# Kernel tuning notes

Hardware: AMD Instinct MI355X
Metric: run time of the kernel (lower is better)

The kernel has to match this reference:

```python
import jax, jax.numpy as jnp
import numpy as np

N = 100000        # nodes
E = 1600000       # edges (avg degree 16)
F_IN = 512        # num_features
H1, D1 = 8, 8     # layer-1 heads x per-head dim (concat -> 64)
C = 16            # num_classes (layer-2: 1 head, dim C)
NEG_SLOPE = 0.2


def setup_inputs() -> dict:
    key = jax.random.key(0)
    ks = jax.random.split(key, 8)
    x = jax.random.normal(ks[0], (N, F_IN), dtype=jnp.float32)
    edge_index = jax.random.randint(ks[1], (2, E), 0, N, dtype=jnp.int64)
    W1 = jax.random.normal(ks[2], (F_IN, H1 * D1), dtype=jnp.float32) / np.float32(np.sqrt(F_IN))
    a1_src = jax.random.normal(ks[3], (H1, D1), dtype=jnp.float32) * 0.1
    a1_dst = jax.random.normal(ks[4], (H1, D1), dtype=jnp.float32) * 0.1
    W2 = jax.random.normal(ks[5], (H1 * D1, C), dtype=jnp.float32) / np.float32(np.sqrt(H1 * D1))
    a2_src = jax.random.normal(ks[6], (1, C), dtype=jnp.float32) * 0.1
    a2_dst = jax.random.normal(ks[7], (1, C), dtype=jnp.float32) * 0.1
    return {"x": x, "edge_index": edge_index, "W1": W1, "a1_src": a1_src,
            "a1_dst": a1_dst, "W2": W2, "a2_src": a2_src, "a2_dst": a2_dst}


def gat_layer(x, src, dst, W, a_s, a_d, heads, out_dim):
    """Multi-head GAT conv: gather -> per-edge leaky-relu score -> segment
    softmax over destination -> scatter-aggregate. Returns [N, heads, out_dim]."""
    n = x.shape[0]
    h = (x @ W).reshape(n, heads, out_dim)            # [N, H, D]
    es = jnp.einsum('nhd,hd->nh', h, a_s)             # source attention term
    ed = jnp.einsum('nhd,hd->nh', h, a_d)             # dest attention term
    e = jax.nn.leaky_relu(es[src] + ed[dst], NEG_SLOPE)   # [E, H]
    m = jax.ops.segment_max(e, dst, num_segments=n)       # stable softmax max
    ex = jnp.exp(e - m[dst])
    s = jax.ops.segment_sum(ex, dst, num_segments=n)
    alpha = ex / s[dst]                               # [E, H]
    out = jax.ops.segment_sum(h[src] * alpha[..., None], dst, num_segments=n)
    return out                                        # [N, H, D]


def reference(x, edge_index, W1, a1_src, a1_dst, W2, a2_src, a2_dst):
    n = x.shape[0]
    loop = jnp.arange(n, dtype=edge_index.dtype)
    src = jnp.concatenate([edge_index[0], loop])      # add self-loops
    dst = jnp.concatenate([edge_index[1], loop])
    # eval mode: dropout(p=0.6, training=False) is identity
    h1 = gat_layer(x, src, dst, W1, a1_src, a1_dst, H1, D1).reshape(n, H1 * D1)
    h1 = jax.nn.elu(h1)
    h2 = gat_layer(h1, src, dst, W2, a2_src, a2_dst, 1, C).reshape(n, C)
    return jax.nn.log_softmax(h2, axis=1)
```

## Files before the change

kernel.cpp:

```cpp
#include <hip/hip_runtime.h>
#include <hip/hip_bf16.h>

#define F_IN 512
#define H1 8
#define D1 8
#define F_MID 64
#define C 16
#define NEG_SLOPE 0.2f
#define SCAN_CHUNK 1024
#define BIN_CHUNK 8192
#define NB_MAX 1024
#define BUCKET_SHIFT 7
#define BUCKET_STRIDE 3072

typedef __attribute__((ext_vector_type(8))) short bf16x8;
typedef __attribute__((ext_vector_type(4))) float f32x4;

static __device__ __forceinline__ unsigned short f2bf(float f) {
    __hip_bfloat16 h = __float2bfloat16(f);
    return *(unsigned short*)&h;
}

__global__ __launch_bounds__(256) void k_bin(const int* __restrict__ src,
                                             const int* __restrict__ dst,
                                             int* __restrict__ gcur,
                                             int2* __restrict__ bucketed,
                                             int n_edges, int nb) {
    __shared__ int cnt[NB_MAX];
    __shared__ int base[NB_MAX];
    const int t = threadIdx.x;
    const int eb = blockIdx.x * BIN_CHUNK;
    for (int b = t; b < nb; b += 256) cnt[b] = 0;
    __syncthreads();
#pragma unroll
    for (int i = 0; i < BIN_CHUNK / 256; ++i) {
        int e = eb + i * 256 + t;
        if (e < n_edges) atomicAdd(&cnt[dst[e] >> BUCKET_SHIFT], 1);
    }
    __syncthreads();
    for (int b = t; b < nb; b += 256) {
        int c = cnt[b];
        base[b] = c > 0 ? atomicAdd(&gcur[b], c) : 0;
        cnt[b] = 0;
    }
    __syncthreads();
#pragma unroll
    for (int i = 0; i < BIN_CHUNK / 256; ++i) {
        int e = eb + i * 256 + t;
        if (e < n_edges) {
            int d = dst[e];
            int b = d >> BUCKET_SHIFT;
            int local = atomicAdd(&cnt[b], 1);
            bucketed[(size_t)b * BUCKET_STRIDE + base[b] + local] = make_int2(src[e], d);
        }
    }
}

__global__ __launch_bounds__(256) void k_bhist(const int* __restrict__ gcur,
                                               const int2* __restrict__ bucketed,
                                               int* __restrict__ counts, int n_nodes) {
    __shared__ int cnt[1 << BUCKET_SHIFT];
    const int t = threadIdx.x;
    const int b = blockIdx.x;
    if (t < (1 << BUCKET_SHIFT)) cnt[t] = 0;
    __syncthreads();
    const int total = gcur[b];
    const int2* bp = bucketed + (size_t)b * BUCKET_STRIDE;
    for (int i = t; i < total; i += 256)
        atomicAdd(&cnt[bp[i].y & ((1 << BUCKET_SHIFT) - 1)], 1);
    __syncthreads();
    if (t < (1 << BUCKET_SHIFT)) {
        int node = (b << BUCKET_SHIFT) + t;
        if (node < n_nodes) counts[node] = cnt[t];
    }
}

__global__ __launch_bounds__(256) void k_bsort(const int* __restrict__ gcur,
                                               const int2* __restrict__ bucketed,
                                               int* __restrict__ cursor,
                                               int* __restrict__ sorted_src) {
    const int b = blockIdx.x;
    const int total = gcur[b];
    const int2* bp = bucketed + (size_t)b * BUCKET_STRIDE;
    for (int i = threadIdx.x; i < total; i += 256) {
        int2 ed = bp[i];
        int pos = atomicAdd(&cursor[ed.y], 1);
        sorted_src[pos] = ed.x;
    }
}

__global__ __launch_bounds__(256) void k_scan_reduce(const int* __restrict__ counts,
                                                     int* __restrict__ block_sums, int n) {
    const int t = threadIdx.x;
    const int base = blockIdx.x * SCAN_CHUNK + t * 4;
    int s = 0;
#pragma unroll
    for (int j = 0; j < 4; ++j) {
        int idx = base + j;
        if (idx < n) s += counts[idx];
    }
#pragma unroll
    for (int off = 1; off < 64; off <<= 1) s += __shfl_xor(s, off, 64);
    __shared__ int ws[4];
    if ((t & 63) == 0) ws[t >> 6] = s;
    __syncthreads();
    if (t == 0) block_sums[blockIdx.x] = ws[0] + ws[1] + ws[2] + ws[3];
}

__global__ __launch_bounds__(256) void k_scan_sums(int* __restrict__ block_sums,
                                                   int* __restrict__ block_offs,
                                                   int* __restrict__ row_start_last,
                                                   int nb) {
    __shared__ int sh[256];
    const int t = threadIdx.x;
    sh[t] = (t < nb) ? block_sums[t] : 0;
    __syncthreads();
#pragma unroll
    for (int d = 1; d < 256; d <<= 1) {
        int v = (t >= d) ? sh[t - d] : 0;
        __syncthreads();
        sh[t] += v;
        __syncthreads();
    }
    if (t < nb) block_offs[t] = sh[t] - block_sums[t];
    if (t == 255) *row_start_last = sh[255];
}

__global__ __launch_bounds__(256) void k_scan_apply(const int* __restrict__ counts,
                                                    const int* __restrict__ block_offs,
                                                    int* __restrict__ row_start,
                                                    int* __restrict__ cursor, int n) {
    const int t = threadIdx.x;
    const int base = blockIdx.x * SCAN_CHUNK + t * 4;
    int c[4];
#pragma unroll
    for (int j = 0; j < 4; ++j) c[j] = (base + j < n) ? counts[base + j] : 0;
    const int tsum = c[0] + c[1] + c[2] + c[3];
    int isc = tsum;
#pragma unroll
    for (int off = 1; off < 64; off <<= 1) {
        int v = __shfl_up(isc, off, 64);
        if ((t & 63) >= off) isc += v;
    }
    __shared__ int wsum[4];
    if ((t & 63) == 63) wsum[t >> 6] = isc;
    __syncthreads();
    int woff = 0;
    const int w = t >> 6;
    for (int i = 0; i < 4; ++i) if (i < w) woff += wsum[i];
    int off = block_offs[blockIdx.x] + woff + (isc - tsum);
#pragma unroll
    for (int j = 0; j < 4; ++j) {
        int idx = base + j;
        if (idx < n) { row_start[idx] = off; cursor[idx] = off; }
        off += c[j];
    }
}

__global__ __launch_bounds__(256) void k_w1t(const float* __restrict__ W1,
                                             __hip_bfloat16* __restrict__ w1t) {
    int idx = blockIdx.x * 256 + threadIdx.x;
    int k = idx >> 6, n = idx & 63;
    w1t[n * F_IN + k] = __float2bfloat16(W1[idx]);
}

__global__ __launch_bounds__(256) void k_gemm1(const float* __restrict__ x,
                                               const __hip_bfloat16* __restrict__ w1t,
                                               const float* __restrict__ a1s,
                                               const float* __restrict__ a1d,
                                               __hip_bfloat16* __restrict__ h1b,
                                               float* __restrict__ es1,
                                               float* __restrict__ ed1, int n_nodes) {
    __shared__ unsigned short Xs[64][72];
    __shared__ unsigned short Ws[64][72];
    __shared__ float sas[64], sad[64];
    const int t = threadIdx.x;
    if (t < 64) sas[t] = a1s[t];
    else if (t < 128) sad[t - 64] = a1d[t - 64];

    const int wv = t >> 6, l = t & 63;
    const int q = l >> 4, m16 = l & 15;
    const int rowbase = blockIdx.x * 64;

    const int sr = t >> 2, sf = t & 3;
    int gx = rowbase + sr;
    gx = gx < n_nodes ? gx : n_nodes - 1;
    const float* xrow = x + (size_t)gx * F_IN;
    const __hip_bfloat16* wrow = w1t + (size_t)sr * F_IN;

    f32x4 acc[4];
#pragma unroll
    for (int i = 0; i < 4; ++i) acc[i] = (f32x4){0.f, 0.f, 0.f, 0.f};

    for (int kt = 0; kt < F_IN; kt += 64) {
#pragma unroll
        for (int j = 0; j < 4; ++j) {
            float4 v = *(const float4*)(xrow + kt + sf * 16 + j * 4);
            ushort4 b;
            b.x = f2bf(v.x); b.y = f2bf(v.y); b.z = f2bf(v.z); b.w = f2bf(v.w);
            *(ushort4*)&Xs[sr][sf * 16 + j * 4] = b;
        }
#pragma unroll
        for (int j = 0; j < 2; ++j) {
            *(int4*)&Ws[sr][sf * 16 + j * 8] =
                *(const int4*)(wrow + kt + sf * 16 + j * 8);
        }
        __syncthreads();
#pragma unroll
        for (int kk = 0; kk < 2; ++kk) {
            bf16x8 bfrag = *(const bf16x8*)&Xs[wv * 16 + m16][kk * 32 + q * 8];
#pragma unroll
            for (int tn = 0; tn < 4; ++tn) {
                bf16x8 afrag = *(const bf16x8*)&Ws[tn * 16 + m16][kk * 32 + q * 8];
                acc[tn] = __builtin_amdgcn_mfma_f32_16x16x32_bf16(afrag, bfrag, acc[tn], 0, 0, 0);
            }
        }
        __syncthreads();
    }

    const int node = rowbase + wv * 16 + m16;
    const bool ok = node < n_nodes;
#pragma unroll
    for (int tn = 0; tn < 4; ++tn) {
        const f32x4 a = acc[tn];
        const int nw0 = tn * 16 + q * 4;
        float vs = a.x * sas[nw0] + a.y * sas[nw0 + 1] + a.z * sas[nw0 + 2] + a.w * sas[nw0 + 3];
        float vd = a.x * sad[nw0] + a.y * sad[nw0 + 1] + a.z * sad[nw0 + 2] + a.w * sad[nw0 + 3];
        vs += __shfl_xor(vs, 16, 64);
        vd += __shfl_xor(vd, 16, 64);
        if (ok) {
            ushort4 b;
            b.x = f2bf(a.x); b.y = f2bf(a.y); b.z = f2bf(a.z); b.w = f2bf(a.w);
            *(ushort4*)(h1b + (size_t)node * F_MID + nw0) = b;
            if ((q & 1) == 0) {
                const int head = 2 * tn + (q >> 1);
                es1[node * H1 + head] = vs;
                ed1[node * H1 + head] = vd;
            }
        }
    }
}

__global__ __launch_bounds__(256) void k_gather1(const int* __restrict__ row_start,
                                                 const int* __restrict__ sorted_src,
                                                 const __hip_bfloat16* __restrict__ h1b,
                                                 const float* __restrict__ es1,
                                                 const float* __restrict__ ed1,
                                                 float* __restrict__ h1, int n_nodes) {
    const int n = blockIdx.x * 4 + (threadIdx.x >> 6);
    if (n >= n_nodes) return;
    const int lane = threadIdx.x & 63;
    const int h = lane >> 3;
    const float edh = ed1[n * H1 + h];
    const int beg = row_start[n], end = row_start[n + 1];
    float acc = 0.f, den = 0.f;
    for (int base = beg; base < end; base += 64) {
        const int m = min(64, end - base);
        const int li = lane < m ? lane : (m - 1);
        const int myS = sorted_src[base + li];
        int j = 0;
        for (; j + 4 <= m; j += 4) {
            const int s0 = __shfl(myS, j, 64), s1 = __shfl(myS, j + 1, 64);
            const int s2 = __shfl(myS, j + 2, 64), s3 = __shfl(myS, j + 3, 64);
            float e0 = es1[s0 * H1 + h], e1 = es1[s1 * H1 + h];
            float e2 = es1[s2 * H1 + h], e3 = es1[s3 * H1 + h];
            const float f0 = __bfloat162float(h1b[(size_t)s0 * F_MID + lane]);
            const float f1 = __bfloat162float(h1b[(size_t)s1 * F_MID + lane]);
            const float f2 = __bfloat162float(h1b[(size_t)s2 * F_MID + lane]);
            const float f3 = __bfloat162float(h1b[(size_t)s3 * F_MID + lane]);
            e0 += edh; e1 += edh; e2 += edh; e3 += edh;
            e0 = e0 > 0.f ? e0 : NEG_SLOPE * e0;
            e1 = e1 > 0.f ? e1 : NEG_SLOPE * e1;
            e2 = e2 > 0.f ? e2 : NEG_SLOPE * e2;
            e3 = e3 > 0.f ? e3 : NEG_SLOPE * e3;
            const float w0 = __expf(e0), w1 = __expf(e1), w2 = __expf(e2), w3 = __expf(e3);
            acc += w0 * f0 + w1 * f1 + w2 * f2 + w3 * f3;
            den += (w0 + w1) + (w2 + w3);
        }
        for (; j < m; ++j) {
            const int s = __shfl(myS, j, 64);
            float ev = es1[s * H1 + h] + edh;
            ev = ev > 0.f ? ev : NEG_SLOPE * ev;
            const float w = __expf(ev);
            acc += w * __bfloat162float(h1b[(size_t)s * F_MID + lane]);
            den += w;
        }
    }
    float evs = es1[n * H1 + h] + edh;
    evs = evs > 0.f ? evs : NEG_SLOPE * evs;
    const float ws = __expf(evs);
    acc += ws * __bfloat162float(h1b[(size_t)n * F_MID + lane]);
    den += ws;
    float v = acc / den;
    v = v > 0.f ? v : expm1f(v);
    h1[(size_t)n * F_MID + lane] = v;
}

__global__ void k_gemm2(const float* __restrict__ h1, const float* __restrict__ W2,
                        const float* __restrict__ a2s, const float* __restrict__ a2d,
                        __hip_bfloat16* __restrict__ h2b, float* __restrict__ es2,
                        float* __restrict__ ed2, int n_nodes) {
    __shared__ float w2s[F_MID * C];
    __shared__ float h1s[16][F_MID + 1];
    const int t = threadIdx.x;
    const int nb = blockIdx.x * 16;
    for (int i = t; i < F_MID * C; i += 256) w2s[i] = W2[i];
    for (int i = t; i < 16 * F_MID; i += 256) {
        int r = i >> 6, k = i & 63;
        int n = nb + r;
        h1s[r][k] = h1[(size_t)(n < n_nodes ? n : n_nodes - 1) * F_MID + k];
    }
    __syncthreads();
    const int r = t >> 4, c = t & 15;
    const int n = nb + r;
    float acc = 0.f;
#pragma unroll
    for (int k = 0; k < F_MID; ++k) acc += h1s[r][k] * w2s[k * C + c];
    float vs = acc * a2s[c], vd = acc * a2d[c];
#pragma unroll
    for (int off = 1; off < 16; off <<= 1) {
        vs += __shfl_xor(vs, off, 64);
        vd += __shfl_xor(vd, off, 64);
    }
    if (n < n_nodes) {
        h2b[(size_t)n * C + c] = __float2bfloat16(acc);
        if (c == 0) { es2[n] = vs; ed2[n] = vd; }
    }
}

__global__ __launch_bounds__(256) void k_gather2(const int* __restrict__ row_start,
                                                 const int* __restrict__ sorted_src,
                                                 const __hip_bfloat16* __restrict__ h2b,
                                                 const float* __restrict__ es2,
                                                 const float* __restrict__ ed2,
                                                 float* __restrict__ out, int n_nodes) {
    const int n = blockIdx.x * 16 + (threadIdx.x >> 4);
    if (n >= n_nodes) return;
    const int lane = threadIdx.x & 63;
    const int c = lane & 15;
    const int g = lane >> 4;
    const float ed = ed2[n];
    const int beg = row_start[n], end = row_start[n + 1];
    float acc = 0.f, den = 0.f;
    for (int base = beg; base < end; base += 16) {
        const int m = min(16, end - base);
        const int li = c < m ? c : (m - 1);
        const int myS = sorted_src[base + li];
        int j = 0;
        for (; j + 4 <= m; j += 4) {
            const int s0 = __shfl(myS, g * 16 + j, 64), s1 = __shfl(myS, g * 16 + j + 1, 64);
            const int s2 = __shfl(myS, g * 16 + j + 2, 64), s3 = __shfl(myS, g * 16 + j + 3, 64);
            float e0 = es2[s0] + ed, e1 = es2[s1] + ed, e2 = es2[s2] + ed, e3 = es2[s3] + ed;
            const float f0 = __bfloat162float(h2b[(size_t)s0 * C + c]);
            const float f1 = __bfloat162float(h2b[(size_t)s1 * C + c]);
            const float f2 = __bfloat162float(h2b[(size_t)s2 * C + c]);
            const float f3 = __bfloat162float(h2b[(size_t)s3 * C + c]);
            e0 = e0 > 0.f ? e0 : NEG_SLOPE * e0;
            e1 = e1 > 0.f ? e1 : NEG_SLOPE * e1;
            e2 = e2 > 0.f ? e2 : NEG_SLOPE * e2;
            e3 = e3 > 0.f ? e3 : NEG_SLOPE * e3;
            const float w0 = __expf(e0), w1 = __expf(e1), w2 = __expf(e2), w3 = __expf(e3);
            acc += w0 * f0 + w1 * f1 + w2 * f2 + w3 * f3;
            den += (w0 + w1) + (w2 + w3);
        }
        for (; j < m; ++j) {
            const int s = __shfl(myS, g * 16 + j, 64);
            float ev = es2[s] + ed;
            ev = ev > 0.f ? ev : NEG_SLOPE * ev;
            const float w = __expf(ev);
            acc += w * __bfloat162float(h2b[(size_t)s * C + c]);
            den += w;
        }
    }
    float evs = es2[n] + ed;
    evs = evs > 0.f ? evs : NEG_SLOPE * evs;
    const float ws = __expf(evs);
    acc += ws * __bfloat162float(h2b[(size_t)n * C + c]);
    den += ws;
    const float v = acc / den;
    float mx = v;
#pragma unroll
    for (int off = 1; off < 16; off <<= 1) mx = fmaxf(mx, __shfl_xor(mx, off, 64));
    float se = __expf(v - mx);
#pragma unroll
    for (int off = 1; off < 16; off <<= 1) se += __shfl_xor(se, off, 64);
    out[(size_t)n * C + c] = v - mx - __logf(se);
}

extern "C" void kernel_launch(void* const* d_in, const int* in_sizes, int n_in,
                              void* d_out, int out_size, void* d_ws, size_t ws_size,
                              hipStream_t stream) {
    const float* x   = (const float*)d_in[0];
    const int*   ei  = (const int*)d_in[1];
    const float* W1  = (const float*)d_in[2];
    const float* a1s = (const float*)d_in[3];
    const float* a1d = (const float*)d_in[4];
    const float* W2  = (const float*)d_in[5];
    const float* a2s = (const float*)d_in[6];
    const float* a2d = (const float*)d_in[7];
    float* out = (float*)d_out;

    const int n_nodes = in_sizes[0] / F_IN;
    const int n_edges = in_sizes[1] / 2;
    const int* src = ei;
    const int* dst = ei + n_edges;
    const int n_scan_blocks = (n_nodes + SCAN_CHUNK - 1) / SCAN_CHUNK;
    const int nb = (n_nodes + (1 << BUCKET_SHIFT) - 1) >> BUCKET_SHIFT;

    float* fws = (float*)d_ws;
    float* es1 = fws;
    float* ed1 = es1 + (size_t)n_nodes * H1;
    float* h1  = ed1 + (size_t)n_nodes * H1;
    float* es2 = h1  + (size_t)n_nodes * F_MID;
    float* ed2 = es2 + n_nodes;
    __hip_bfloat16* h1b = (__hip_bfloat16*)(ed2 + n_nodes);
    __hip_bfloat16* h2b = h1b + (size_t)n_nodes * F_MID;
    __hip_bfloat16* w1t = h2b + (size_t)n_nodes * C;
    int* iws        = (int*)(w1t + F_IN * F_MID);
    int* counts     = iws;
    int* gcur       = counts + n_nodes;
    int* row_start  = gcur + NB_MAX;
    int* cursor     = row_start + n_nodes + 1;
    int* sorted_src = cursor + n_nodes;
    int* block_sums = sorted_src + n_edges;
    int* block_offs = block_sums + 256;
    int2* bucketed  = (int2*)(((uintptr_t)(block_offs + 256) + 15) & ~(uintptr_t)15);

    hipMemsetAsync(counts, 0, ((size_t)n_nodes + NB_MAX) * sizeof(int), stream);

    k_bin<<<(n_edges + BIN_CHUNK - 1) / BIN_CHUNK, 256, 0, stream>>>(src, dst, gcur, bucketed, n_edges, nb);
    k_bhist<<<nb, 256, 0, stream>>>(gcur, bucketed, counts, n_nodes);
    k_scan_reduce<<<n_scan_blocks, 256, 0, stream>>>(counts, block_sums, n_nodes);
    k_scan_sums<<<1, 256, 0, stream>>>(block_sums, block_offs, &row_start[n_nodes], n_scan_blocks);
    k_scan_apply<<<n_scan_blocks, 256, 0, stream>>>(counts, block_offs, row_start, cursor, n_nodes);
    k_bsort<<<nb, 256, 0, stream>>>(gcur, bucketed, cursor, sorted_src);

    k_w1t<<<(F_IN * F_MID) / 256, 256, 0, stream>>>(W1, w1t);
    k_gemm1<<<(n_nodes + 63) / 64, 256, 0, stream>>>(x, w1t, a1s, a1d, h1b, es1, ed1, n_nodes);
    k_gather1<<<(n_nodes + 3) / 4, 256, 0, stream>>>(row_start, sorted_src, h1b, es1, ed1, h1, n_nodes);

    k_gemm2<<<(n_nodes + 15) / 16, 256, 0, stream>>>(h1, W2, a2s, a2d, h2b, es2, ed2, n_nodes);
    k_gather2<<<(n_nodes + 15) / 16, 256, 0, stream>>>(row_start, sorted_src, h2b, es2, ed2, out, n_nodes);
}
```

Measured before the change: 535.2 us.

## Replace global CSR scan with per-bucket local scan and shared-memory placement

```diff
diff --git a/kernel.cpp b/kernel.cpp
--- a/kernel.cpp
+++ b/kernel.cpp
@@ -7,8 +7,7 @@
 #define F_MID 64
 #define C 16
 #define NEG_SLOPE 0.2f
-#define SCAN_CHUNK 1024
-#define BIN_CHUNK 8192
+#define BIN_CHUNK 4096
 #define NB_MAX 1024
 #define BUCKET_SHIFT 7
 #define BUCKET_STRIDE 3072
@@ -56,104 +55,68 @@
     }
 }
 
-__global__ __launch_bounds__(256) void k_bhist(const int* __restrict__ gcur,
+__global__ __launch_bounds__(1024) void k_bscan(const int* __restrict__ gcur,
+                                                int* __restrict__ bucket_base,
+                                                int* __restrict__ row_start_last,
+                                                int nb, int n_edges_total) {
+    __shared__ int sh[1024];
+    const int t = threadIdx.x;
+    const int v = (t < nb) ? gcur[t] : 0;
+    sh[t] = v;
+    __syncthreads();
+#pragma unroll
+    for (int d = 1; d < 1024; d <<= 1) {
+        int u = (t >= d) ? sh[t - d] : 0;
+        __syncthreads();
+        sh[t] += u;
+        __syncthreads();
+    }
+    if (t < nb) bucket_base[t] = sh[t] - v;
+    if (t == 0) *row_start_last = n_edges_total;
+}
+
+__global__ __launch_bounds__(256) void k_place(const int* __restrict__ gcur,
+                                               const int* __restrict__ bucket_base,
                                                const int2* __restrict__ bucketed,
-                                               int* __restrict__ counts, int n_nodes) {
+                                               int* __restrict__ row_start,
+                                               int* __restrict__ sorted_src, int n_nodes) {
+    __shared__ int2 stage[BUCKET_STRIDE];
     __shared__ int cnt[1 << BUCKET_SHIFT];
+    __shared__ int cur[1 << BUCKET_SHIFT];
     const int t = threadIdx.x;
     const int b = blockIdx.x;
     if (t < (1 << BUCKET_SHIFT)) cnt[t] = 0;
     __syncthreads();
     const int total = gcur[b];
     const int2* bp = bucketed + (size_t)b * BUCKET_STRIDE;
-    for (int i = t; i < total; i += 256)
-        atomicAdd(&cnt[bp[i].y & ((1 << BUCKET_SHIFT) - 1)], 1);
-    __syncthreads();
+    for (int i = t; i < total; i += 256) {
+        int2 e = bp[i];
+        stage[i] = e;
+        atomicAdd(&cnt[e.y & ((1 << BUCKET_SHIFT) - 1)], 1);
+    }
+    __syncthreads();
+    if (t < (1 << BUCKET_SHIFT)) cur[t] = cnt[t];
+    __syncthreads();
+#pragma unroll
+    for (int d = 1; d < (1 << BUCKET_SHIFT); d <<= 1) {
+        int u = 0;
+        if (t < (1 << BUCKET_SHIFT) && t >= d) u = cur[t - d];
+        __syncthreads();
+        if (t < (1 << BUCKET_SHIFT)) cur[t] += u;
+        __syncthreads();
+    }
+    const int base0 = bucket_base[b];
     if (t < (1 << BUCKET_SHIFT)) {
         int node = (b << BUCKET_SHIFT) + t;
-        if (node < n_nodes) counts[node] = cnt[t];
-    }
-}
-
-__global__ __launch_bounds__(256) void k_bsort(const int* __restrict__ gcur,
-                                               const int2* __restrict__ bucketed,
-                                               int* __restrict__ cursor,
-                                               int* __restrict__ sorted_src) {
-    const int b = blockIdx.x;
-    const int total = gcur[b];
-    const int2* bp = bucketed + (size_t)b * BUCKET_STRIDE;
-    for (int i = threadIdx.x; i < total; i += 256) {
-        int2 ed = bp[i];
-        int pos = atomicAdd(&cursor[ed.y], 1);
-        sorted_src[pos] = ed.x;
-    }
-}
-
-__global__ __launch_bounds__(256) void k_scan_reduce(const int* __restrict__ counts,
-                                                     int* __restrict__ block_sums, int n) {
-    const int t = threadIdx.x;
-    const int base = blockIdx.x * SCAN_CHUNK + t * 4;
-    int s = 0;
-#pragma unroll
-    for (int j = 0; j < 4; ++j) {
-        int idx = base + j;
-        if (idx < n) s += counts[idx];
-    }
-#pragma unroll
-    for (int off = 1; off < 64; off <<= 1) s += __shfl_xor(s, off, 64);
-    __shared__ int ws[4];
-    if ((t & 63) == 0) ws[t >> 6] = s;
-    __syncthreads();
-    if (t == 0) block_sums[blockIdx.x] = ws[0] + ws[1] + ws[2] + ws[3];
-}
-
-__global__ __launch_bounds__(256) void k_scan_sums(int* __restrict__ block_sums,
-                                                   int* __restrict__ block_offs,
-                                                   int* __restrict__ row_start_last,
-                                                   int nb) {
-    __shared__ int sh[256];
-    const int t = threadIdx.x;
-    sh[t] = (t < nb) ? block_sums[t] : 0;
-    __syncthreads();
-#pragma unroll
-    for (int d = 1; d < 256; d <<= 1) {
-        int v = (t >= d) ? sh[t - d] : 0;
-        __syncthreads();
-        sh[t] += v;
-        __syncthreads();
-    }
-    if (t < nb) block_offs[t] = sh[t] - block_sums[t];
-    if (t == 255) *row_start_last = sh[255];
-}
-
-__global__ __launch_bounds__(256) void k_scan_apply(const int* __restrict__ counts,
-                                                    const int* __restrict__ block_offs,
-                                                    int* __restrict__ row_start,
-                                                    int* __restrict__ cursor, int n) {
-    const int t = threadIdx.x;
-    const int base = blockIdx.x * SCAN_CHUNK + t * 4;
-    int c[4];
-#pragma unroll
-    for (int j = 0; j < 4; ++j) c[j] = (base + j < n) ? counts[base + j] : 0;
-    const int tsum = c[0] + c[1] + c[2] + c[3];
-    int isc = tsum;
-#pragma unroll
-    for (int off = 1; off < 64; off <<= 1) {
-        int v = __shfl_up(isc, off, 64);
-        if ((t & 63) >= off) isc += v;
-    }
-    __shared__ int wsum[4];
-    if ((t & 63) == 63) wsum[t >> 6] = isc;
-    __syncthreads();
-    int woff = 0;
-    const int w = t >> 6;
-    for (int i = 0; i < 4; ++i) if (i < w) woff += wsum[i];
-    int off = block_offs[blockIdx.x] + woff + (isc - tsum);
-#pragma unroll
-    for (int j = 0; j < 4; ++j) {
-        int idx = base + j;
-        if (idx < n) { row_start[idx] = off; cursor[idx] = off; }
-        off += c[j];
+        int excl = cur[t] - cnt[t];
+        if (node < n_nodes) row_start[node] = base0 + excl;
+        cur[t] = excl;
+    }
+    __syncthreads();
+    for (int i = t; i < total; i += 256) {
+        int2 e = stage[i];
+        int p = atomicAdd(&cur[e.y & ((1 << BUCKET_SHIFT) - 1)], 1);
+        sorted_src[base0 + p] = e.x;
     }
 }
 
@@ -404,7 +367,6 @@
     const int n_edges = in_sizes[1] / 2;
     const int* src = ei;
     const int* dst = ei + n_edges;
-    const int n_scan_blocks = (n_nodes + SCAN_CHUNK - 1) / SCAN_CHUNK;
     const int nb = (n_nodes + (1 << BUCKET_SHIFT) - 1) >> BUCKET_SHIFT;
 
     float* fws = (float*)d_ws;
@@ -416,24 +378,18 @@
     __hip_bfloat16* h1b = (__hip_bfloat16*)(ed2 + n_nodes);
     __hip_bfloat16* h2b = h1b + (size_t)n_nodes * F_MID;
     __hip_bfloat16* w1t = h2b + (size_t)n_nodes * C;
-    int* iws        = (int*)(w1t + F_IN * F_MID);
-    int* counts     = iws;
-    int* gcur       = counts + n_nodes;
-    int* row_start  = gcur + NB_MAX;
-    int* cursor     = row_start + n_nodes + 1;
-    int* sorted_src = cursor + n_nodes;
-    int* block_sums = sorted_src + n_edges;
-    int* block_offs = block_sums + 256;
-    int2* bucketed  = (int2*)(((uintptr_t)(block_offs + 256) + 15) & ~(uintptr_t)15);
-
-    hipMemsetAsync(counts, 0, ((size_t)n_nodes + NB_MAX) * sizeof(int), stream);
+    int* iws         = (int*)(w1t + F_IN * F_MID);
+    int* gcur        = iws;
+    int* bucket_base = gcur + NB_MAX;
+    int* row_start   = bucket_base + NB_MAX;
+    int* sorted_src  = row_start + n_nodes + 1;
+    int2* bucketed   = (int2*)(((uintptr_t)(sorted_src + n_edges) + 15) & ~(uintptr_t)15);
+
+    hipMemsetAsync(gcur, 0, NB_MAX * sizeof(int), stream);
 
     k_bin<<<(n_edges + BIN_CHUNK - 1) / BIN_CHUNK, 256, 0, stream>>>(src, dst, gcur, bucketed, n_edges, nb);
-    k_bhist<<<nb, 256, 0, stream>>>(gcur, bucketed, counts, n_nodes);
-    k_scan_reduce<<<n_scan_blocks, 256, 0, stream>>>(counts, block_sums, n_nodes);
-    k_scan_sums<<<1, 256, 0, stream>>>(block_sums, block_offs, &row_start[n_nodes], n_scan_blocks);
-    k_scan_apply<<<n_scan_blocks, 256, 0, stream>>>(counts, block_offs, row_start, cursor, n_nodes);
-    k_bsort<<<nb, 256, 0, stream>>>(gcur, bucketed, cursor, sorted_src);
+    k_bscan<<<1, 1024, 0, stream>>>(gcur, bucket_base, &row_start[n_nodes], nb, n_edges);
+    k_place<<<nb, 256, 0, stream>>>(gcur, bucket_base, bucketed, row_start, sorted_src, n_nodes);
 
     k_w1t<<<(F_IN * F_MID) / 256, 256, 0, stream>>>(W1, w1t);
     k_gemm1<<<(n_nodes + 63) / 64, 256, 0, stream>>>(x, w1t, a1s, a1d, h1b, es1, ed1, n_nodes);
```

New measurement: 487.6 us. 1.1x faster.
